# Performance work log

Measured on AMD Instinct MI355X. Metric: run time of the kernel, lower is better.

## Reference

```python
import jax, jax.numpy as jnp
import numpy as np

NEG = -9e15
EPS = 1e-5

def setup_inputs() -> dict:
    key = jax.random.key(0)
    k1, k2, k3, k4 = jax.random.split(key, 4)
    B, S, D = 4, 2048, 1024
    q = jax.random.normal(k1, (B, S, D), dtype=jnp.float32)
    k = jax.random.normal(k2, (B, S, D), dtype=jnp.float32)
    v = jax.random.normal(k3, (B, S, D), dtype=jnp.float32)
    mask = jax.random.randint(k4, (B, S, S), 0, 2, dtype=jnp.int32)
    gamma = jnp.ones((D,), dtype=jnp.float32)
    beta = jnp.zeros((D,), dtype=jnp.float32)
    return {"q": q, "k": k, "v": v, "mask": mask, "gamma": gamma, "beta": beta}

def reference(q, k, v, mask, gamma, beta):
    d_k = q.shape[-1]
    # scaled dot-product attention: [B,S,S] logits materialized as in original
    logits = jnp.einsum('bsd,btd->bst', q, k) / jnp.sqrt(jnp.asarray(d_k, q.dtype))
    logits = jnp.where(mask == 0, jnp.asarray(NEG, logits.dtype), logits)
    attn = jax.nn.softmax(logits, axis=-1)
    x = jnp.einsum('bst,btd->bsd', attn, v)
    # dropout is identity at inference; LayerNorm over last dim
    mu = jnp.mean(x, axis=-1, keepdims=True)
    var = jnp.mean(jnp.square(x - mu), axis=-1, keepdims=True)
    xhat = (x - mu) * jax.lax.rsqrt(var + EPS)
    return xhat * gamma + beta
```

## Files before the change

### kernel.cpp

```cpp
#include <hip/hip_runtime.h>
#include <hip/hip_bf16.h>

typedef unsigned short u16;
typedef unsigned long long u64;
typedef __attribute__((ext_vector_type(8))) short bf16x8;
typedef __attribute__((ext_vector_type(4))) float f32x4;
typedef __attribute__((ext_vector_type(4))) float float4v;
typedef __attribute__((ext_vector_type(4))) short short4v;
typedef __attribute__((ext_vector_type(4))) int int4v;
typedef __attribute__((ext_vector_type(4))) unsigned int u32x4;
typedef __attribute__((ext_vector_type(4))) unsigned long long u64x4;

#define BB 4
#define SS 2048
#define DD 1024

__device__ __forceinline__ u16 f2bf(float x){
    unsigned u = __float_as_uint(x);
    return (u16)((u + 0x7fffu + ((u >> 16) & 1u)) >> 16);
}

__device__ __forceinline__ unsigned cvtpk(float lo, float hi){
    unsigned r;
    asm("v_cvt_pk_bf16_f32 %0, %1, %2" : "=v"(r) : "v"(lo), "v"(hi));
    return r;
}

#define GLD16(g, l) __builtin_amdgcn_global_load_lds( \
    (const __attribute__((address_space(1))) unsigned int*)(g), \
    (__attribute__((address_space(3))) unsigned int*)(l), 16, 0, 0)

#define SCHED0() __builtin_amdgcn_sched_barrier(0)
#define PH_PRE()  SCHED0(); __builtin_amdgcn_s_barrier(); SCHED0(); __builtin_amdgcn_s_setprio(1)
#define PH_POST() __builtin_amdgcn_s_setprio(0); SCHED0(); __builtin_amdgcn_s_barrier(); SCHED0()

__global__ __launch_bounds__(256) void prep_kernel(
    const float* __restrict__ q, const float* __restrict__ k,
    const float* __restrict__ v, const int* __restrict__ mask,
    u16* __restrict__ Qb, u16* __restrict__ Kb, u16* __restrict__ Vt,
    u64* __restrict__ mbits64, float* __restrict__ rowsum)
{
    const int bid = blockIdx.x;
    const int tid = threadIdx.x;

    if (bid < 4096){
        const float* in = (bid < 2048) ? q : k;
        u16* out = (bid < 2048) ? Qb : Kb;
        const float scale = (bid < 2048) ? 0.03125f : 1.0f;
        const int sb = bid & 2047;
#pragma unroll
        for (int u = 0; u < 2; ++u){
            const int i8 = (sb * 256 + tid) * 2 + u;
            float4v a = ((const float4v*)in)[i8 * 2];
            float4v c = ((const float4v*)in)[i8 * 2 + 1];
            u32x4 w;
            w[0] = cvtpk(a[0] * scale, a[1] * scale);
            w[1] = cvtpk(a[2] * scale, a[3] * scale);
            w[2] = cvtpk(c[0] * scale, c[1] * scale);
            w[3] = cvtpk(c[2] * scale, c[3] * scale);
            ((u32x4*)out)[i8] = w;
        }
    } else if (bid < 6144){
        __shared__ float tile[64][65];
        const int sb = bid - 4096;
        const int b  = sb >> 9;
        const int r  = sb & 511;
        const int s0 = (r >> 4) << 6;
        const int d0 = (r & 15) << 6;
        const int tx = tid & 15;
        const int ty = tid >> 4;
#pragma unroll
        for (int kk = 0; kk < 4; ++kk){
            const float* p = v + ((size_t)(b * SS + s0 + ty + 16 * kk) * DD) + d0 + tx * 4;
            float4v val = *(const float4v*)p;
            tile[ty + 16 * kk][tx * 4 + 0] = val[0];
            tile[ty + 16 * kk][tx * 4 + 1] = val[1];
            tile[ty + 16 * kk][tx * 4 + 2] = val[2];
            tile[ty + 16 * kk][tx * 4 + 3] = val[3];
        }
        __syncthreads();
#pragma unroll
        for (int u = 0; u < 2; ++u){
            const int unit = u * 256 + tid;
            const int d  = unit & 63;
            const int sg = unit >> 6;
            u32x4 w;
            w[0] = cvtpk(tile[sg * 8 + 0][d], tile[sg * 8 + 1][d]);
            w[1] = cvtpk(tile[sg * 8 + 2][d], tile[sg * 8 + 3][d]);
            w[2] = cvtpk(tile[sg * 8 + 4][d], tile[sg * 8 + 5][d]);
            w[3] = cvtpk(tile[sg * 8 + 6][d], tile[sg * 8 + 7][d]);
            *(u32x4*)&Vt[((size_t)(b * DD + d0 + d) * SS) + s0 + sg * 8] = w;
        }
    } else if (bid < 8192){
        const int sb = bid - 6144;
        const int tt = sb * 256 + tid;
        const int lane = tid & 63;
#pragma unroll
        for (int j = 0; j < 8; ++j){
            const int idx = j * 524288 + tt;
            int4v mm = ((const int4v*)mask)[idx];
            u64 b0 = __ballot(mm[0] != 0);
            u64 b1 = __ballot(mm[1] != 0);
            u64 b2 = __ballot(mm[2] != 0);
            u64 b3 = __ballot(mm[3] != 0);
            const int gw = idx >> 6;
            if (lane < 4){
                u64 w = (lane == 0) ? b0 : (lane == 1) ? b1 : (lane == 2) ? b2 : b3;
                mbits64[(size_t)gw * 4 + lane] = w;
            }
        }
    } else {
        rowsum[(bid - 8192) * 256 + tid] = 0.f;
    }
}

__global__ __launch_bounds__(512) void qk_kernel(
    const u16* __restrict__ Qb, const u16* __restrict__ Kb,
    const u64* __restrict__ mbits64, u16* __restrict__ P,
    float* __restrict__ rowsum)
{
    __shared__ __align__(16) u16 As[2][256 * 64];
    __shared__ __align__(16) u16 Bs[2][256 * 64];

    const int swz = ((blockIdx.x & 7) << 5) + (blockIdx.x >> 3);
    const int b   = swz >> 6;
    const int bx  = (swz >> 3) & 7;
    const int by  = swz & 7;
    const int row0 = bx << 8, col0 = by << 8;

    const int tid = threadIdx.x;
    const int wid = tid >> 6, lane = tid & 63;
    const int l16 = lane & 15, g4 = lane >> 4;
    const int wq = wid >> 2, wk = wid & 3;

    const int sr   = tid >> 3;
    const int scol = ((tid & 7) ^ (sr & 7)) << 3;
    const u16* gA = Kb + (size_t)(b * SS + col0 + sr) * DD + scol;
    const u16* gB = Qb + (size_t)(b * SS + row0 + sr) * DD + scol;
    char* const lA0 = (char*)As[0] + tid * 16;
    char* const lB0 = (char*)Bs[0] + tid * 16;
    char* const lA1 = (char*)As[1] + tid * 16;
    char* const lB1 = (char*)Bs[1] + tid * 16;

    const int kRow = (wk * 64  + l16) << 7;
    const int qRow = (wq * 128 + l16) << 7;
    const int cx0  = (g4 << 4) ^ ((l16 & 7) << 4);

    f32x4 acc[4][8];
    const f32x4 z4 = {0.f, 0.f, 0.f, 0.f};
#pragma unroll
    for (int i = 0; i < 4; ++i)
#pragma unroll
        for (int j = 0; j < 8; ++j) acc[i][j] = z4;

#define STAGE_QK(kt, la, lb) { \
    const u16* ga_ = gA + (kt) * 64; \
    const u16* gb_ = gB + (kt) * 64; \
    GLD16(ga_,            (la)); \
    GLD16(ga_ +  64 * DD, (la) + 8192); \
    GLD16(ga_ + 128 * DD, (la) + 16384); \
    GLD16(ga_ + 192 * DD, (la) + 24576); \
    GLD16(gb_,            (lb)); \
    GLD16(gb_ +  64 * DD, (lb) + 8192); \
    GLD16(gb_ + 128 * DD, (lb) + 16384); \
    GLD16(gb_ + 192 * DD, (lb) + 24576); }

#define LDQ8(Bb_, kx) { \
    const char* p_ = (const char*)(Bb_) + qRow + ((kx) ? (cx0 ^ 64) : cx0); \
    fq0 = *(const bf16x8*)(p_);          fq1 = *(const bf16x8*)(p_ + 2048); \
    fq2 = *(const bf16x8*)(p_ + 4096);   fq3 = *(const bf16x8*)(p_ + 6144); \
    fq4 = *(const bf16x8*)(p_ + 8192);   fq5 = *(const bf16x8*)(p_ + 10240); \
    fq6 = *(const bf16x8*)(p_ + 12288);  fq7 = *(const bf16x8*)(p_ + 14336); }

#define LDK2(Ab_, mh, kx) { \
    const char* p_ = (const char*)(Ab_) + kRow + (mh) * 4096 + ((kx) ? (cx0 ^ 64) : cx0); \
    fk0 = *(const bf16x8*)(p_); \
    fk1 = *(const bf16x8*)(p_ + 2048); }

#define MKROW(mi, fk) \
    acc[mi][0] = __builtin_amdgcn_mfma_f32_16x16x32_bf16(fk, fq0, acc[mi][0],0,0,0); \
    acc[mi][1] = __builtin_amdgcn_mfma_f32_16x16x32_bf16(fk, fq1, acc[mi][1],0,0,0); \
    acc[mi][2] = __builtin_amdgcn_mfma_f32_16x16x32_bf16(fk, fq2, acc[mi][2],0,0,0); \
    acc[mi][3] = __builtin_amdgcn_mfma_f32_16x16x32_bf16(fk, fq3, acc[mi][3],0,0,0); \
    acc[mi][4] = __builtin_amdgcn_mfma_f32_16x16x32_bf16(fk, fq4, acc[mi][4],0,0,0); \
    acc[mi][5] = __builtin_amdgcn_mfma_f32_16x16x32_bf16(fk, fq5, acc[mi][5],0,0,0); \
    acc[mi][6] = __builtin_amdgcn_mfma_f32_16x16x32_bf16(fk, fq6, acc[mi][6],0,0,0); \
    acc[mi][7] = __builtin_amdgcn_mfma_f32_16x16x32_bf16(fk, fq7, acc[mi][7],0,0,0);

    STAGE_QK(0, lA0, lB0);
    STAGE_QK(1, lA1, lB1);
    asm volatile("s_waitcnt vmcnt(8)" ::: "memory");
    SCHED0(); __builtin_amdgcn_s_barrier(); SCHED0();

#pragma unroll 1
    for (int it = 0; it < 8; ++it){
        bf16x8 fq0, fq1, fq2, fq3, fq4, fq5, fq6, fq7, fk0, fk1;
        LDK2(As[0], 0, 0); LDQ8(Bs[0], 0);
        PH_PRE(); MKROW(0,fk0) MKROW(1,fk1) PH_POST();
        LDK2(As[0], 1, 0);
        PH_PRE(); MKROW(2,fk0) MKROW(3,fk1) PH_POST();
        LDK2(As[0], 0, 1); LDQ8(Bs[0], 1);
        PH_PRE(); MKROW(0,fk0) MKROW(1,fk1) PH_POST();
        LDK2(As[0], 1, 1);
        PH_PRE(); MKROW(2,fk0) MKROW(3,fk1) PH_POST();
        if (it < 7){
            STAGE_QK(2*it+2, lA0, lB0);
            asm volatile("s_waitcnt vmcnt(8)" ::: "memory");
        } else {
            asm volatile("s_waitcnt vmcnt(0)" ::: "memory");
        }
        SCHED0(); __builtin_amdgcn_s_barrier(); SCHED0();
        LDK2(As[1], 0, 0); LDQ8(Bs[1], 0);
        PH_PRE(); MKROW(0,fk0) MKROW(1,fk1) PH_POST();
        LDK2(As[1], 1, 0);
        PH_PRE(); MKROW(2,fk0) MKROW(3,fk1) PH_POST();
        LDK2(As[1], 0, 1); LDQ8(Bs[1], 1);
        PH_PRE(); MKROW(0,fk0) MKROW(1,fk1) PH_POST();
        LDK2(As[1], 1, 1);
        PH_PRE(); MKROW(2,fk0) MKROW(3,fk1) PH_POST();
        if (it < 7){
            STAGE_QK(2*it+3, lA1, lB1);
            asm volatile("s_waitcnt vmcnt(8)" ::: "memory");
            SCHED0(); __builtin_amdgcn_s_barrier(); SCHED0();
        }
    }
#undef STAGE_QK
#undef LDQ8
#undef LDK2
#undef MKROW

#pragma unroll
    for (int nq = 0; nq < 8; ++nq){
        const int grow = row0 + wq * 128 + nq * 16 + l16;
        const size_t rbase = (size_t)(b * SS + grow) * SS;
        u64x4 w = *(const u64x4*)&mbits64[((size_t)(b * SS + grow) * 8 + by) * 4];
        float rs = 0.f;
#pragma unroll
        for (int mk = 0; mk < 4; ++mk){
            const int sh = wk * 16 + mk * 4 + g4;
            const int gcolb = col0 + wk * 64 + mk * 16 + g4 * 4;
            float e0 = ((w[0] >> sh) & 1ull) ? __expf(acc[mk][nq][0]) : 0.f;
            float e1 = ((w[1] >> sh) & 1ull) ? __expf(acc[mk][nq][1]) : 0.f;
            float e2 = ((w[2] >> sh) & 1ull) ? __expf(acc[mk][nq][2]) : 0.f;
            float e3 = ((w[3] >> sh) & 1ull) ? __expf(acc[mk][nq][3]) : 0.f;
            short4v pp;
            pp[0] = (short)f2bf(e0); pp[1] = (short)f2bf(e1);
            pp[2] = (short)f2bf(e2); pp[3] = (short)f2bf(e3);
            *(short4v*)&P[rbase + gcolb] = pp;
            rs += (e0 + e1) + (e2 + e3);
        }
        rs += __shfl_xor(rs, 16);
        rs += __shfl_xor(rs, 32);
        if (g4 == 0) atomicAdd(&rowsum[b * SS + grow], rs);
    }
}

__global__ __launch_bounds__(512, 2) void pv_kernel(
    const u16* __restrict__ P, const u16* __restrict__ Vt,
    const float* __restrict__ rowsum, u16* __restrict__ Xn)
{
    __shared__ __align__(16) u16 As[2][128 * 64];
    __shared__ __align__(16) u16 Bs[2][256 * 64];

    const int swz = ((blockIdx.x & 7) << 5) + (blockIdx.x >> 3);
    const int b   = swz >> 6;
    const int bx  = (swz >> 2) & 15;
    const int by  = swz & 3;
    const int row0 = bx << 7, col0 = by << 8;

    const int tid = threadIdx.x;
    const int wid = tid >> 6, lane = tid & 63;
    const int l16 = lane & 15, g4 = lane >> 4;
    const int wr = wid >> 2, wc = wid & 3;

    const int sr   = tid >> 3;
    const int scol = ((tid & 7) ^ (sr & 7)) << 3;
    const u16* gA = P  + (size_t)(b * SS + row0 + sr) * SS + scol;
    const u16* gB = Vt + (size_t)(b * DD + col0 + sr) * SS + scol;
    char* const lA0 = (char*)As[0] + tid * 16;
    char* const lB0 = (char*)Bs[0] + tid * 16;
    char* const lA1 = (char*)As[1] + tid * 16;
    char* const lB1 = (char*)Bs[1] + tid * 16;

    const int aRow = (wr * 64 + l16) << 7;
    const int bRow = (wc * 64 + l16) << 7;
    const int cx0  = (g4 << 4) ^ ((l16 & 7) << 4);

    f32x4 acc[4][4];
    const f32x4 z4 = {0.f, 0.f, 0.f, 0.f};
#pragma unroll
    for (int i = 0; i < 4; ++i)
#pragma unroll
        for (int j = 0; j < 4; ++j) acc[i][j] = z4;

#define STAGE_PV(kt, la, lb) { \
    const u16* ga_ = gA + (kt) * 64; \
    const u16* gb_ = gB + (kt) * 64; \
    GLD16(ga_,            (la)); \
    GLD16(ga_ +  64 * SS, (la) + 8192); \
    GLD16(gb_,            (lb)); \
    GLD16(gb_ +  64 * SS, (lb) + 8192); \
    GLD16(gb_ + 128 * SS, (lb) + 16384); \
    GLD16(gb_ + 192 * SS, (lb) + 24576); }

#define LDA2(Ab_, mh, kx) { \
    const char* p_ = (const char*)(Ab_) + aRow + (mh) * 4096 + ((kx) ? (cx0 ^ 64) : cx0); \
    fa0 = *(const bf16x8*)(p_); \
    fa1 = *(const bf16x8*)(p_ + 2048); }

#define LDB4(Bb_, kx) { \
    const char* p_ = (const char*)(Bb_) + bRow + ((kx) ? (cx0 ^ 64) : cx0); \
    fb0 = *(const bf16x8*)(p_); \
    fb1 = *(const bf16x8*)(p_ + 2048); \
    fb2 = *(const bf16x8*)(p_ + 4096); \
    fb3 = *(const bf16x8*)(p_ + 6144); }

#define MROWP(mi, fa) \
    acc[mi][0] = __builtin_amdgcn_mfma_f32_16x16x32_bf16(fa, fb0, acc[mi][0],0,0,0); \
    acc[mi][1] = __builtin_amdgcn_mfma_f32_16x16x32_bf16(fa, fb1, acc[mi][1],0,0,0); \
    acc[mi][2] = __builtin_amdgcn_mfma_f32_16x16x32_bf16(fa, fb2, acc[mi][2],0,0,0); \
    acc[mi][3] = __builtin_amdgcn_mfma_f32_16x16x32_bf16(fa, fb3, acc[mi][3],0,0,0);

    STAGE_PV(0, lA0, lB0);
    STAGE_PV(1, lA1, lB1);
    asm volatile("s_waitcnt vmcnt(6)" ::: "memory");
    SCHED0(); __builtin_amdgcn_s_barrier(); SCHED0();

#pragma unroll 1
    for (int it = 0; it < 16; ++it){
        bf16x8 fa0, fa1, fb0, fb1, fb2, fb3;
        LDA2(As[0], 0, 0); LDB4(Bs[0], 0);
        PH_PRE(); MROWP(0,fa0) MROWP(1,fa1) PH_POST();
        LDA2(As[0], 1, 0);
        PH_PRE(); MROWP(2,fa0) MROWP(3,fa1) PH_POST();
        LDA2(As[0], 0, 1); LDB4(Bs[0], 1);
        PH_PRE(); MROWP(0,fa0) MROWP(1,fa1) PH_POST();
        LDA2(As[0], 1, 1);
        PH_PRE(); MROWP(2,fa0) MROWP(3,fa1) PH_POST();
        if (it < 15){
            STAGE_PV(2*it+2, lA0, lB0);
            asm volatile("s_waitcnt vmcnt(6)" ::: "memory");
        } else {
            asm volatile("s_waitcnt vmcnt(0)" ::: "memory");
        }
        SCHED0(); __builtin_amdgcn_s_barrier(); SCHED0();
        LDA2(As[1], 0, 0); LDB4(Bs[1], 0);
        PH_PRE(); MROWP(0,fa0) MROWP(1,fa1) PH_POST();
        LDA2(As[1], 1, 0);
        PH_PRE(); MROWP(2,fa0) MROWP(3,fa1) PH_POST();
        LDA2(As[1], 0, 1); LDB4(Bs[1], 1);
        PH_PRE(); MROWP(0,fa0) MROWP(1,fa1) PH_POST();
        LDA2(As[1], 1, 1);
        PH_PRE(); MROWP(2,fa0) MROWP(3,fa1) PH_POST();
        if (it < 15){
            STAGE_PV(2*it+3, lA1, lB1);
            asm volatile("s_waitcnt vmcnt(6)" ::: "memory");
            SCHED0(); __builtin_amdgcn_s_barrier(); SCHED0();
        }
    }
#undef STAGE_PV
#undef LDA2
#undef LDB4
#undef MROWP

#pragma unroll
    for (int m = 0; m < 4; ++m){
        float inv[4];
#pragma unroll
        for (int r = 0; r < 4; ++r)
            inv[r] = 1.f / rowsum[b * SS + row0 + wr * 64 + m * 16 + g4 * 4 + r];
#pragma unroll
        for (int n = 0; n < 4; ++n){
            const int gcol = col0 + wc * 64 + n * 16 + l16;
#pragma unroll
            for (int r = 0; r < 4; ++r){
                const int grow = row0 + wr * 64 + m * 16 + g4 * 4 + r;
                Xn[(size_t)(b * SS + grow) * DD + gcol] = f2bf(acc[m][n][r] * inv[r]);
            }
        }
    }
}

__global__ __launch_bounds__(256) void ln_kernel(
    const u16* __restrict__ Xn, const float* __restrict__ gamma,
    const float* __restrict__ beta, float* __restrict__ out)
{
    __shared__ float red[2][4];
    const int row = blockIdx.x;
    const int t = threadIdx.x;
    short4v xv = *(const short4v*)&Xn[(size_t)row * DD + t * 4];
    float x[4];
#pragma unroll
    for (int j = 0; j < 4; ++j)
        x[j] = __uint_as_float(((unsigned)(u16)xv[j]) << 16);
    float s  = x[0] + x[1] + x[2] + x[3];
    float sq = x[0]*x[0] + x[1]*x[1] + x[2]*x[2] + x[3]*x[3];
#pragma unroll
    for (int d = 1; d < 64; d <<= 1){ s += __shfl_xor(s, d); sq += __shfl_xor(sq, d); }
    const int wv = t >> 6;
    if ((t & 63) == 0){ red[0][wv] = s; red[1][wv] = sq; }
    __syncthreads();
    float S  = red[0][0] + red[0][1] + red[0][2] + red[0][3];
    float Sq = red[1][0] + red[1][1] + red[1][2] + red[1][3];
    float mu = S * (1.f / 1024.f);
    float var = Sq * (1.f / 1024.f) - mu * mu;
    float rstd = rsqrtf(var + 1e-5f);
    float4v g  = *(const float4v*)&gamma[t * 4];
    float4v be = *(const float4v*)&beta[t * 4];
    float4v o;
#pragma unroll
    for (int j = 0; j < 4; ++j) o[j] = (x[j] - mu) * rstd * g[j] + be[j];
    *(float4v*)&out[(size_t)row * DD + t * 4] = o;
}

extern "C" void kernel_launch(void* const* d_in, const int* in_sizes, int n_in,
                              void* d_out, int out_size, void* d_ws, size_t ws_size,
                              hipStream_t stream) {
    const float* q     = (const float*)d_in[0];
    const float* k     = (const float*)d_in[1];
    const float* v     = (const float*)d_in[2];
    const int*   mask  = (const int*)d_in[3];
    const float* gamma = (const float*)d_in[4];
    const float* beta  = (const float*)d_in[5];
    float* out = (float*)d_out;

    u16* Qb = (u16*)d_ws;
    u16* Kb = Qb + (size_t)BB * SS * DD;
    u16* Vt = Kb + (size_t)BB * SS * DD;
    u16* P  = Vt + (size_t)BB * SS * DD;
    u16* Xn = P  + (size_t)BB * SS * SS;
    float* rowsum = (float*)(Xn + (size_t)BB * SS * DD);
    u64* mbits64 = (u64*)Xn;

    prep_kernel<<<8224, 256, 0, stream>>>(q, k, v, mask, Qb, Kb, Vt, mbits64, rowsum);
    qk_kernel<<<256, 512, 0, stream>>>(Qb, Kb, mbits64, P, rowsum);
    pv_kernel<<<256, 512, 0, stream>>>(P, Vt, rowsum, Xn);
    ln_kernel<<<BB * SS, 256, 0, stream>>>(Xn, gamma, beta, out);
}
```

Baseline: 142.2 us.

## Halve QK tile along KV to 128x256 and run two blocks per CU

The QK GEMM tile shrinks from 256x256 to 128 KV by 256 Q rows, which doubles the grid to 512 blocks and cuts per-wave accumulators from 32 to 16 MFMA tiles. Launch bounds now request 2 blocks per CU, and the LDS staging and wait counts are adjusted to match. The aim is better occupancy and CU coverage on a device with 256 CUs, so that some blocks can hide latency while others compute. In exchange, each Q tile is loaded twice as often, so the arithmetic intensity per block drops.

```diff
diff --git a/kernel.cpp b/kernel.cpp
--- a/kernel.cpp
+++ b/kernel.cpp
@@ -114,131 +114,126 @@
     }
 }
 
-__global__ __launch_bounds__(512) void qk_kernel(
+__global__ __launch_bounds__(512, 2) void qk_kernel(
     const u16* __restrict__ Qb, const u16* __restrict__ Kb,
     const u64* __restrict__ mbits64, u16* __restrict__ P,
     float* __restrict__ rowsum)
 {
-    __shared__ __align__(16) u16 As[2][256 * 64];
+    __shared__ __align__(16) u16 As[2][128 * 64];
     __shared__ __align__(16) u16 Bs[2][256 * 64];
 
-    const int swz = ((blockIdx.x & 7) << 5) + (blockIdx.x >> 3);
-    const int b   = swz >> 6;
-    const int bx  = (swz >> 3) & 7;
-    const int by  = swz & 7;
-    const int row0 = bx << 8, col0 = by << 8;
+    const int swz = ((blockIdx.x & 7) << 6) + (blockIdx.x >> 3);
+    const int b   = swz >> 7;
+    const int bkv = (swz >> 3) & 15;
+    const int bq  = swz & 7;
+    const int kv0 = bkv << 7, q0 = bq << 8;
 
     const int tid = threadIdx.x;
     const int wid = tid >> 6, lane = tid & 63;
     const int l16 = lane & 15, g4 = lane >> 4;
-    const int wq = wid >> 2, wk = wid & 3;
+    const int wr = wid >> 2, wc = wid & 3;
 
     const int sr   = tid >> 3;
     const int scol = ((tid & 7) ^ (sr & 7)) << 3;
-    const u16* gA = Kb + (size_t)(b * SS + col0 + sr) * DD + scol;
-    const u16* gB = Qb + (size_t)(b * SS + row0 + sr) * DD + scol;
+    const u16* gA = Kb + (size_t)(b * SS + kv0 + sr) * DD + scol;
+    const u16* gB = Qb + (size_t)(b * SS + q0  + sr) * DD + scol;
     char* const lA0 = (char*)As[0] + tid * 16;
     char* const lB0 = (char*)Bs[0] + tid * 16;
     char* const lA1 = (char*)As[1] + tid * 16;
     char* const lB1 = (char*)Bs[1] + tid * 16;
 
-    const int kRow = (wk * 64  + l16) << 7;
-    const int qRow = (wq * 128 + l16) << 7;
+    const int aRow = (wr * 64 + l16) << 7;
+    const int bRow = (wc * 64 + l16) << 7;
     const int cx0  = (g4 << 4) ^ ((l16 & 7) << 4);
 
-    f32x4 acc[4][8];
+    f32x4 acc[4][4];
     const f32x4 z4 = {0.f, 0.f, 0.f, 0.f};
 #pragma unroll
     for (int i = 0; i < 4; ++i)
 #pragma unroll
-        for (int j = 0; j < 8; ++j) acc[i][j] = z4;
+        for (int j = 0; j < 4; ++j) acc[i][j] = z4;
 
 #define STAGE_QK(kt, la, lb) { \
     const u16* ga_ = gA + (kt) * 64; \
     const u16* gb_ = gB + (kt) * 64; \
     GLD16(ga_,            (la)); \
     GLD16(ga_ +  64 * DD, (la) + 8192); \
-    GLD16(ga_ + 128 * DD, (la) + 16384); \
-    GLD16(ga_ + 192 * DD, (la) + 24576); \
     GLD16(gb_,            (lb)); \
     GLD16(gb_ +  64 * DD, (lb) + 8192); \
     GLD16(gb_ + 128 * DD, (lb) + 16384); \
     GLD16(gb_ + 192 * DD, (lb) + 24576); }
 
-#define LDQ8(Bb_, kx) { \
-    const char* p_ = (const char*)(Bb_) + qRow + ((kx) ? (cx0 ^ 64) : cx0); \
-    fq0 = *(const bf16x8*)(p_);          fq1 = *(const bf16x8*)(p_ + 2048); \
-    fq2 = *(const bf16x8*)(p_ + 4096);   fq3 = *(const bf16x8*)(p_ + 6144); \
-    fq4 = *(const bf16x8*)(p_ + 8192);   fq5 = *(const bf16x8*)(p_ + 10240); \
-    fq6 = *(const bf16x8*)(p_ + 12288);  fq7 = *(const bf16x8*)(p_ + 14336); }
-
-#define LDK2(Ab_, mh, kx) { \
-    const char* p_ = (const char*)(Ab_) + kRow + (mh) * 4096 + ((kx) ? (cx0 ^ 64) : cx0); \
-    fk0 = *(const bf16x8*)(p_); \
-    fk1 = *(const bf16x8*)(p_ + 2048); }
-
-#define MKROW(mi, fk) \
-    acc[mi][0] = __builtin_amdgcn_mfma_f32_16x16x32_bf16(fk, fq0, acc[mi][0],0,0,0); \
-    acc[mi][1] = __builtin_amdgcn_mfma_f32_16x16x32_bf16(fk, fq1, acc[mi][1],0,0,0); \
-    acc[mi][2] = __builtin_amdgcn_mfma_f32_16x16x32_bf16(fk, fq2, acc[mi][2],0,0,0); \
-    acc[mi][3] = __builtin_amdgcn_mfma_f32_16x16x32_bf16(fk, fq3, acc[mi][3],0,0,0); \
-    acc[mi][4] = __builtin_amdgcn_mfma_f32_16x16x32_bf16(fk, fq4, acc[mi][4],0,0,0); \
-    acc[mi][5] = __builtin_amdgcn_mfma_f32_16x16x32_bf16(fk, fq5, acc[mi][5],0,0,0); \
-    acc[mi][6] = __builtin_amdgcn_mfma_f32_16x16x32_bf16(fk, fq6, acc[mi][6],0,0,0); \
-    acc[mi][7] = __builtin_amdgcn_mfma_f32_16x16x32_bf16(fk, fq7, acc[mi][7],0,0,0);
+#define LDA2(Ab_, mh, kx) { \
+    const char* p_ = (const char*)(Ab_) + aRow + (mh) * 4096 + ((kx) ? (cx0 ^ 64) : cx0); \
+    fa0 = *(const bf16x8*)(p_); \
+    fa1 = *(const bf16x8*)(p_ + 2048); }
+
+#define LDB4(Bb_, kx) { \
+    const char* p_ = (const char*)(Bb_) + bRow + ((kx) ? (cx0 ^ 64) : cx0); \
+    fb0 = *(const bf16x8*)(p_); \
+    fb1 = *(const bf16x8*)(p_ + 2048); \
+    fb2 = *(const bf16x8*)(p_ + 4096); \
+    fb3 = *(const bf16x8*)(p_ + 6144); }
+
+#define MROWQ(mi, fa) \
+    acc[mi][0] = __builtin_amdgcn_mfma_f32_16x16x32_bf16(fa, fb0, acc[mi][0],0,0,0); \
+    acc[mi][1] = __builtin_amdgcn_mfma_f32_16x16x32_bf16(fa, fb1, acc[mi][1],0,0,0); \
+    acc[mi][2] = __builtin_amdgcn_mfma_f32_16x16x32_bf16(fa, fb2, acc[mi][2],0,0,0); \
+    acc[mi][3] = __builtin_amdgcn_mfma_f32_16x16x32_bf16(fa, fb3, acc[mi][3],0,0,0);
 
     STAGE_QK(0, lA0, lB0);
     STAGE_QK(1, lA1, lB1);
-    asm volatile("s_waitcnt vmcnt(8)" ::: "memory");
+    asm volatile("s_waitcnt vmcnt(6)" ::: "memory");
     SCHED0(); __builtin_amdgcn_s_barrier(); SCHED0();
 
 #pragma unroll 1
     for (int it = 0; it < 8; ++it){
-        bf16x8 fq0, fq1, fq2, fq3, fq4, fq5, fq6, fq7, fk0, fk1;
-        LDK2(As[0], 0, 0); LDQ8(Bs[0], 0);
-        PH_PRE(); MKROW(0,fk0) MKROW(1,fk1) PH_POST();
-        LDK2(As[0], 1, 0);
-        PH_PRE(); MKROW(2,fk0) MKROW(3,fk1) PH_POST();
-        LDK2(As[0], 0, 1); LDQ8(Bs[0], 1);
-        PH_PRE(); MKROW(0,fk0) MKROW(1,fk1) PH_POST();
-        LDK2(As[0], 1, 1);
-        PH_PRE(); MKROW(2,fk0) MKROW(3,fk1) PH_POST();
+        bf16x8 fa0, fa1, fb0, fb1, fb2, fb3;
+        LDA2(As[0], 0, 0); LDB4(Bs[0], 0);
+        PH_PRE(); MROWQ(0,fa0) MROWQ(1,fa1) PH_POST();
+        LDA2(As[0], 1, 0);
+        PH_PRE(); MROWQ(2,fa0) MROWQ(3,fa1) PH_POST();
+        LDA2(As[0], 0, 1); LDB4(Bs[0], 1);
+        PH_PRE(); MROWQ(0,fa0) MROWQ(1,fa1) PH_POST();
+        LDA2(As[0], 1, 1);
+        PH_PRE(); MROWQ(2,fa0) MROWQ(3,fa1) PH_POST();
         if (it < 7){
             STAGE_QK(2*it+2, lA0, lB0);
-            asm volatile("s_waitcnt vmcnt(8)" ::: "memory");
+            asm volatile("s_waitcnt vmcnt(6)" ::: "memory");
         } else {
             asm volatile("s_waitcnt vmcnt(0)" ::: "memory");
         }
         SCHED0(); __builtin_amdgcn_s_barrier(); SCHED0();
-        LDK2(As[1], 0, 0); LDQ8(Bs[1], 0);
-        PH_PRE(); MKROW(0,fk0) MKROW(1,fk1) PH_POST();
-        LDK2(As[1], 1, 0);
-        PH_PRE(); MKROW(2,fk0) MKROW(3,fk1) PH_POST();
-        LDK2(As[1], 0, 1); LDQ8(Bs[1], 1);
-        PH_PRE(); MKROW(0,fk0) MKROW(1,fk1) PH_POST();
-        LDK2(As[1], 1, 1);
-        PH_PRE(); MKROW(2,fk0) MKROW(3,fk1) PH_POST();
+        LDA2(As[1], 0, 0); LDB4(Bs[1], 0);
+        PH_PRE(); MROWQ(0,fa0) MROWQ(1,fa1) PH_POST();
+        LDA2(As[1], 1, 0);
+        PH_PRE(); MROWQ(2,fa0) MROWQ(3,fa1) PH_POST();
+        LDA2(As[1], 0, 1); LDB4(Bs[1], 1);
+        PH_PRE(); MROWQ(0,fa0) MROWQ(1,fa1) PH_POST();
+        LDA2(As[1], 1, 1);
+        PH_PRE(); MROWQ(2,fa0) MROWQ(3,fa1) PH_POST();
         if (it < 7){
             STAGE_QK(2*it+3, lA1, lB1);
-            asm volatile("s_waitcnt vmcnt(8)" ::: "memory");
+            asm volatile("s_waitcnt vmcnt(6)" ::: "memory");
             SCHED0(); __builtin_amdgcn_s_barrier(); SCHED0();
         }
     }
 #undef STAGE_QK
-#undef LDQ8
-#undef LDK2
-#undef MKROW
-
-#pragma unroll
-    for (int nq = 0; nq < 8; ++nq){
-        const int grow = row0 + wq * 128 + nq * 16 + l16;
+#undef LDA2
+#undef LDB4
+#undef MROWQ
+
+    const int shb = ((bkv & 1) << 5) + (wr << 4) + g4;
+#pragma unroll
+    for (int nq = 0; nq < 4; ++nq){
+        const int grow = q0 + wc * 64 + nq * 16 + l16;
         const size_t rbase = (size_t)(b * SS + grow) * SS;
-        u64x4 w = *(const u64x4*)&mbits64[((size_t)(b * SS + grow) * 8 + by) * 4];
+        u64x4 w = *(const u64x4*)&mbits64[((size_t)(b * SS + grow) * 8 + (bkv >> 1)) * 4];
         float rs = 0.f;
 #pragma unroll
         for (int mk = 0; mk < 4; ++mk){
-            const int sh = wk * 16 + mk * 4 + g4;
-            const int gcolb = col0 + wk * 64 + mk * 16 + g4 * 4;
+            const int sh = shb + (mk << 2);
+            const int gcolb = kv0 + wr * 64 + mk * 16 + g4 * 4;
             float e0 = ((w[0] >> sh) & 1ull) ? __expf(acc[mk][nq][0]) : 0.f;
             float e1 = ((w[1] >> sh) & 1ull) ? __expf(acc[mk][nq][1]) : 0.f;
             float e2 = ((w[2] >> sh) & 1ull) ? __expf(acc[mk][nq][2]) : 0.f;
@@ -433,7 +428,7 @@
     u64* mbits64 = (u64*)Xn;
 
     prep_kernel<<<8224, 256, 0, stream>>>(q, k, v, mask, Qb, Kb, Vt, mbits64, rowsum);
-    qk_kernel<<<256, 512, 0, stream>>>(Qb, Kb, mbits64, P, rowsum);
+    qk_kernel<<<512, 512, 0, stream>>>(Qb, Kb, mbits64, P, rowsum);
     pv_kernel<<<256, 512, 0, stream>>>(P, Vt, rowsum, Xn);
     ln_kernel<<<BB * SS, 256, 0, stream>>>(Xn, gamma, beta, out);
 }
```

Result: slower. 150.7 us (+6.0%).
